# Optimization experiments

Hardware: AMD Instinct MI355X
Metric: run time of the kernel (lower is better)

The kernel has to match this reference:

```python
import jax, jax.numpy as jnp
import numpy as np

B, T, D, H = 256, 200, 128, 128


def setup_inputs() -> dict:
    key = jax.random.key(0)
    ks = jax.random.split(key, 6)
    return {
        "x": jax.random.normal(ks[0], (B, T, D), dtype=jnp.float32),
        "duration": jax.random.uniform(ks[1], (B, T), dtype=jnp.float32),
        "rep_indicies": jax.random.randint(ks[2], (B,), 0, T),
        "W_x": jax.random.normal(ks[3], (D, 7 * H), dtype=jnp.float32) / np.float32(np.sqrt(D)),
        "W_h": jax.random.normal(ks[4], (H, 7 * H), dtype=jnp.float32) / np.float32(np.sqrt(H)),
        "b": jnp.zeros((7 * H,), dtype=jnp.float32),
    }


def _ctlstm(x, duration, W_x, W_h, b):
    # Neural-Hawkes continuous-time LSTM scan. x:[B,T,D], duration:[B,T]
    xg = jnp.einsum("btd,dg->btg", x, W_x) + b  # [B,T,7H] precomputed input gates

    def step(carry, inputs):
        h, c_t, cbar = carry  # each [B,H]
        xg_t, dt = inputs     # [B,7H], [B]
        g = xg_t + h @ W_h
        i, f, z, o, ibar, fbar, d = jnp.split(g, 7, axis=-1)
        i, f, o = jax.nn.sigmoid(i), jax.nn.sigmoid(f), jax.nn.sigmoid(o)
        ibar, fbar = jax.nn.sigmoid(ibar), jax.nn.sigmoid(fbar)
        z = jnp.tanh(z)
        delta = jax.nn.softplus(d)
        c = f * c_t + i * z               # cell right after the event
        cbar_new = fbar * cbar + ibar * z  # target cell it decays toward
        c_new = cbar_new + (c - cbar_new) * jnp.exp(-delta * dt[:, None])
        h_new = o * jnp.tanh(c_new)
        return (h_new, c_new, cbar_new), (h_new, c_new)

    z0 = jnp.zeros((x.shape[0], W_h.shape[0]), dtype=x.dtype)
    _, (h_seq, c_seq) = jax.lax.scan(
        step, (z0, z0, z0), (jnp.swapaxes(xg, 0, 1), jnp.swapaxes(duration, 0, 1))
    )
    # h_seq/c_seq: [T,B,H] -> [B,T,H]
    return jnp.swapaxes(h_seq, 0, 1), jnp.swapaxes(c_seq, 0, 1)


def _gather_state(s, rep_indicies):
    # s:[B,T,H]; pick per-sample time index -> [1,B,H]
    idx = jnp.broadcast_to(rep_indicies[:, None, None], (s.shape[0], 1, s.shape[2]))
    return jnp.take_along_axis(s, idx, axis=1)[:, 0, :][None]


def reference(x, duration, rep_indicies, W_x, W_h, b):
    # Dropout is identity in eval mode.
    h_seq, c_seq = _ctlstm(x, duration, W_x, W_h, b)
    return (_gather_state(h_seq, rep_indicies), _gather_state(c_seq, rep_indicies))
```

## Files before the change

### kernel.cpp

```cpp
#include <hip/hip_runtime.h>

#define TT 200
#define BB 256
#define DD 128
#define HH 128
#define NG 896
#define NGP 1024
#define NGP2 1032
#define CH 16

typedef _Float16 half8 __attribute__((ext_vector_type(8)));
typedef _Float16 half4 __attribute__((ext_vector_type(4)));
typedef float float4v __attribute__((ext_vector_type(4)));
typedef int int4v __attribute__((ext_vector_type(4)));

__device__ __forceinline__ float rcpf_(float x) { return __builtin_amdgcn_rcpf(x); }
__device__ __forceinline__ float sigmoidf_(float x) { return rcpf_(1.f + __expf(-x)); }
__device__ __forceinline__ float tanhf_(float x) { return 1.f - 2.f * rcpf_(__expf(2.f * x) + 1.f); }
__device__ __forceinline__ float softplusf_(float x) {
  return fmaxf(x, 0.f) + 0.69314718056f * __log2f(1.f + __expf(-fabsf(x)));
}

__global__ __launch_bounds__(256) void prep_k(const float* __restrict__ Wx,
    const float* __restrict__ Wh, _Float16* __restrict__ WxTp,
    char* __restrict__ WhQ, float* __restrict__ wscale) {
  int bx = blockIdx.x, tid = threadIdx.x;
  if (bx < 28) {
    __shared__ _Float16 Tld[32][136];
    int j0 = bx * 32;
    int jo = tid & 31, kb = tid >> 5;
#pragma unroll
    for (int it = 0; it < 16; ++it) {
      int k = kb + it * 8;
      Tld[jo][k] = (_Float16)Wx[(size_t)k * NG + j0 + jo];
    }
    __syncthreads();
    int g = j0 >> 7, u0 = j0 & 127;
    int jw = tid >> 3, kq = (tid & 7) * 16;
    int pcol = (u0 + jw) * 8 + g;
    *(half8*)&WxTp[(size_t)pcol * DD + kq] = *(const half8*)&Tld[jw][kq];
    *(half8*)&WxTp[(size_t)pcol * DD + kq + 8] = *(const half8*)&Tld[jw][kq + 8];
    return;
  }
  __shared__ float redmax[4][64];
  int c = tid & 63, kq = tid >> 6;
  int col = (bx - 28) * 64 + c;
  float v[32];
  float m = 0.f;
#pragma unroll
  for (int i = 0; i < 32; ++i) {
    v[i] = Wh[(size_t)(kq * 32 + i) * NG + col];
    m = fmaxf(m, fabsf(v[i]));
  }
  redmax[kq][c] = m;
  __syncthreads();
  float mm = fmaxf(fmaxf(redmax[0][c], redmax[1][c]),
                   fmaxf(redmax[2][c], redmax[3][c]));
  mm = mm > 0.f ? mm : 1.f;
  float inv = 127.f * rcpf_(mm);
  char q[32];
#pragma unroll
  for (int i = 0; i < 32; ++i) q[i] = (char)__float2int_rn(v[i] * inv);
#pragma unroll
  for (int i = 0; i < 8; ++i)
    *(int*)&WhQ[(size_t)col * DD + kq * 32 + i * 4] = *(int*)&q[i * 4];
  if (kq == 0) wscale[col] = mm * (1.f / 127.f);
}

__global__ __launch_bounds__(512, 2) void rec_k(const float* __restrict__ x,
    const float* __restrict__ dur, const int* __restrict__ rep,
    const _Float16* __restrict__ WxTp, const char* __restrict__ WhQ,
    const float* __restrict__ wscale, const float* __restrict__ bias,
    float* __restrict__ out) {
  int b = blockIdx.x, j = threadIdx.x;
  int tend = rep[b];
  __shared__ __align__(16) _Float16 xgL[2][CH][NGP2];
  __shared__ __align__(16) _Float16 xld[CH][DD + 8];
  __shared__ __align__(16) char hq[2][HH];
  __shared__ float dlds[TT];
  int w = j >> 6, l = j & 63, lr = l & 15, lg = l >> 4;
  int u = w * 16 + lr;

  int4v wbq[7][2];
  half8 wbx[7][4];
  float sg[7], bias_r[7];
#pragma unroll
  for (int g = 0; g < 7; ++g) {
#pragma unroll
    for (int m = 0; m < 2; ++m)
      wbq[g][m] = *(const int4v*)(WhQ + (size_t)(g * HH + u) * DD + m * 64 + lg * 16);
#pragma unroll
    for (int kk = 0; kk < 4; ++kk)
      wbx[g][kk] = *(const half8*)(WxTp + ((size_t)u * 8 + g) * DD + kk * 32 + lg * 8);
    sg[g] = wscale[g * HH + u] * (1.f / 127.f);
    bias_r[g] = bias[g * HH + u];
  }
  for (int i = j; i < TT; i += 512) dlds[i] = dur[b * TT + i];
  if (lg == 0) { hq[0][u] = (char)0; hq[1][u] = (char)0; }
  float c_s = 0.f, cb_s = 0.f;

  int srow = j >> 5, skq = (j & 31) << 2;
  half8 af[4];
  half8 xo0 = {}, xo1 = {}, xo2 = {}, xo3 = {};
  float4v xraw = (float4v){0.f, 0.f, 0.f, 0.f};

#define PRODG(G)                                                                 \
  do {                                                                           \
    float bv = bias_r[(G)];                                                      \
    float4v pacc = (float4v){bv, bv, bv, bv};                                    \
    _Pragma("unroll") for (int kk = 0; kk < 4; ++kk)                             \
        pacc = __builtin_amdgcn_mfma_f32_16x16x32_f16(af[kk], wbx[(G)][kk],      \
                                                      pacc, 0, 0, 0);            \
    xo0[(G)] = (_Float16)pacc[0];                                                \
    xo1[(G)] = (_Float16)pacc[1];                                                \
    xo2[(G)] = (_Float16)pacc[2];                                                \
    xo3[(G)] = (_Float16)pacc[3];                                                \
  } while (0)

#define XO_WRITE(DST)                                                            \
  do {                                                                           \
    *(half8*)((DST) + (lg * 4 + 0) * NGP2 + u * 8) = xo0;                        \
    *(half8*)((DST) + (lg * 4 + 1) * NGP2 + u * 8) = xo1;                        \
    *(half8*)((DST) + (lg * 4 + 2) * NGP2 + u * 8) = xo2;                        \
    *(half8*)((DST) + (lg * 4 + 3) * NGP2 + u * 8) = xo3;                        \
  } while (0)

  {
    float4v xv = *(const float4v*)(x + ((size_t)b * TT + srow) * DD + skq);
    half4 h4 = {(_Float16)xv[0], (_Float16)xv[1], (_Float16)xv[2], (_Float16)xv[3]};
    *(half4*)&xld[srow][skq] = h4;
  }
  __syncthreads();
#pragma unroll
  for (int kk = 0; kk < 4; ++kk) af[kk] = *(const half8*)&xld[lr][kk * 32 + lg * 8];
  PRODG(0); PRODG(1); PRODG(2); PRODG(3); PRODG(4); PRODG(5); PRODG(6);
  XO_WRITE(&xgL[0][0][0]);
  __syncthreads();

#define PSLICE(S)                                                                \
  do {                                                                           \
    if ((S) == 0) {                                                              \
      int tr = min(base + CH + srow, TT - 1);                                    \
      xraw = *(const float4v*)(x + ((size_t)b * TT + tr) * DD + skq);            \
    } else if ((S) == 1) {                                                       \
      half4 h4 = {(_Float16)xraw[0], (_Float16)xraw[1],                          \
                  (_Float16)xraw[2], (_Float16)xraw[3]};                         \
      *(half4*)&xld[srow][skq] = h4;                                             \
    } else if ((S) == 2) {                                                       \
      _Pragma("unroll") for (int kk = 0; kk < 4; ++kk)                           \
          af[kk] = *(const half8*)&xld[lr][kk * 32 + lg * 8];                    \
    } else if ((S) >= 3 && (S) <= 9) {                                           \
      PRODG((S) - 3);                                                            \
    } else if ((S) == 10) {                                                      \
      XO_WRITE(nb_xg);                                                           \
    }                                                                            \
  } while (0)

#define FSTEP(S)                                                                 \
  if ((S) <= smax) {                                                             \
    if (hasNext) PSLICE(S);                                                      \
    int T = base + (S);                                                          \
    half8 xv = *(const half8*)(cb_xg + (S) * NGP2 + u * 8);                      \
    float dt = dlds[T];                                                          \
    const char* hin = hq[(S) & 1];                                               \
    char* hout = hq[((S) & 1) ^ 1];                                              \
    int4v aq0 = *(const int4v*)&hin[lg * 16];                                    \
    int4v aq1 = *(const int4v*)&hin[64 + lg * 16];                               \
    int4v acc[7];                                                                \
    _Pragma("unroll") for (int g = 0; g < 7; ++g) acc[g] = (int4v){0, 0, 0, 0};  \
    _Pragma("unroll") for (int g = 0; g < 7; ++g)                                \
        acc[g] = __builtin_amdgcn_mfma_i32_16x16x64_i8(aq0, wbq[g][0], acc[g], 0, 0, 0); \
    _Pragma("unroll") for (int g = 0; g < 7; ++g)                                \
        acc[g] = __builtin_amdgcn_mfma_i32_16x16x64_i8(aq1, wbq[g][1], acc[g], 0, 0, 0); \
    float gv[7];                                                                 \
    _Pragma("unroll") for (int g = 0; g < 7; ++g)                                \
        gv[g] = (float)acc[g][0] * sg[g] + (float)xv[g];                         \
    float iv = sigmoidf_(gv[0]), fv = sigmoidf_(gv[1]);                          \
    float zv = tanhf_(gv[2]), ov = sigmoidf_(gv[3]);                             \
    float ibv = sigmoidf_(gv[4]), fbv = sigmoidf_(gv[5]);                        \
    float dv = softplusf_(gv[6]);                                                \
    float cc = fv * c_s + iv * zv;                                               \
    cb_s = fbv * cb_s + ibv * zv;                                                \
    float cn = cb_s + (cc - cb_s) * __expf(-dv * dt);                            \
    float hn = ov * tanhf_(cn);                                                  \
    c_s = cn;                                                                    \
    char hb = (char)__float2int_rn(hn * 127.f);                                  \
    if (lg == 0) {                                                               \
      if (T == tend) {                                                           \
        out[b * HH + u] = hn;                                                    \
        out[BB * HH + b * HH + u] = cn;                                          \
      }                                                                          \
      hout[u] = hb;                                                              \
    }                                                                            \
    __syncthreads();                                                             \
  }

  for (int base = 0; base <= tend; base += CH) {
    int smax = min(CH - 1, tend - base);
    int hasNext = (base + CH) <= tend;
    const _Float16* cb_xg = &xgL[(base >> 4) & 1][0][0];
    _Float16* nb_xg = &xgL[((base >> 4) & 1) ^ 1][0][0];
    FSTEP(0)  FSTEP(1)  FSTEP(2)  FSTEP(3)
    FSTEP(4)  FSTEP(5)  FSTEP(6)  FSTEP(7)
    FSTEP(8)  FSTEP(9)  FSTEP(10) FSTEP(11)
    FSTEP(12) FSTEP(13) FSTEP(14) FSTEP(15)
  }
#undef FSTEP
#undef PSLICE
#undef XO_WRITE
#undef PRODG
}

extern "C" void kernel_launch(void* const* d_in, const int* in_sizes, int n_in,
                              void* d_out, int out_size, void* d_ws, size_t ws_size,
                              hipStream_t stream) {
  const float* x = (const float*)d_in[0];
  const float* dur = (const float*)d_in[1];
  const int* rep = (const int*)d_in[2];
  const float* Wx = (const float*)d_in[3];
  const float* Wh = (const float*)d_in[4];
  const float* bias = (const float*)d_in[5];
  float* out = (float*)d_out;
  char* ws = (char*)d_ws;

  size_t off = 0;
  _Float16* WxTp = (_Float16*)(ws + off); off += (size_t)NGP * DD * 2;
  char* WhQ = (char*)(ws + off); off += (size_t)NG * DD;
  off = (off + 255) & ~(size_t)255;
  float* wscale = (float*)(ws + off); off += (size_t)NG * 4;

  hipLaunchKernelGGL(prep_k, dim3(28 + NG / 64), dim3(256), 0, stream,
                     Wx, Wh, WxTp, WhQ, wscale);
  hipLaunchKernelGGL(rec_k, dim3(BB), dim3(512), 0, stream,
                     x, dur, rep, WxTp, WhQ, wscale, bias, out);
}
```

Before: 162.9 us.

## Stream W_x fragments from global per gate instead of holding them in registers

The 7x4 half8 W_x fragments are no longer kept resident in registers. Two double-buffered fragment sets are now reloaded from global memory (L2-cached) and prefetched one gate ahead inside the pipelined per-step slices. The recurrent int8 MFMA accumulators are also split into a 4-gate and a 3-gate group to shorten register live ranges. The aim is to cut VGPR pressure so the 512x2 launch bound holds without spilling, at the cost of extra global loads on each chunk.

Result: faster. 156.2 us (-4.2%).

```diff
diff --git a/kernel.cpp b/kernel.cpp
--- a/kernel.cpp
+++ b/kernel.cpp
@@ -82,16 +82,12 @@
   int u = w * 16 + lr;
 
   int4v wbq[7][2];
-  half8 wbx[7][4];
   float sg[7], bias_r[7];
 #pragma unroll
   for (int g = 0; g < 7; ++g) {
 #pragma unroll
     for (int m = 0; m < 2; ++m)
       wbq[g][m] = *(const int4v*)(WhQ + (size_t)(g * HH + u) * DD + m * 64 + lg * 16);
-#pragma unroll
-    for (int kk = 0; kk < 4; ++kk)
-      wbx[g][kk] = *(const half8*)(WxTp + ((size_t)u * 8 + g) * DD + kk * 32 + lg * 8);
     sg[g] = wscale[g * HH + u] * (1.f / 127.f);
     bias_r[g] = bias[g * HH + u];
   }
@@ -101,15 +97,23 @@
 
   int srow = j >> 5, skq = (j & 31) << 2;
   half8 af[4];
+  half8 bf0[4], bf1[4];
   half8 xo0 = {}, xo1 = {}, xo2 = {}, xo3 = {};
   float4v xraw = (float4v){0.f, 0.f, 0.f, 0.f};
 
-#define PRODG(G)                                                                 \
+#define WXLOAD(G, BUF)                                                           \
+  do {                                                                           \
+    _Pragma("unroll") for (int kk = 0; kk < 4; ++kk)                             \
+        BUF[kk] = *(const half8*)(WxTp + ((size_t)u * 8 + (G)) * DD +            \
+                                  kk * 32 + lg * 8);                             \
+  } while (0)
+
+#define PRODG(G, BUF)                                                            \
   do {                                                                           \
     float bv = bias_r[(G)];                                                      \
     float4v pacc = (float4v){bv, bv, bv, bv};                                    \
     _Pragma("unroll") for (int kk = 0; kk < 4; ++kk)                             \
-        pacc = __builtin_amdgcn_mfma_f32_16x16x32_f16(af[kk], wbx[(G)][kk],      \
+        pacc = __builtin_amdgcn_mfma_f32_16x16x32_f16(af[kk], BUF[kk],           \
                                                       pacc, 0, 0, 0);            \
     xo0[(G)] = (_Float16)pacc[0];                                                \
     xo1[(G)] = (_Float16)pacc[1];                                                \
@@ -133,7 +137,13 @@
   __syncthreads();
 #pragma unroll
   for (int kk = 0; kk < 4; ++kk) af[kk] = *(const half8*)&xld[lr][kk * 32 + lg * 8];
-  PRODG(0); PRODG(1); PRODG(2); PRODG(3); PRODG(4); PRODG(5); PRODG(6);
+  WXLOAD(0, bf0); PRODG(0, bf0);
+  WXLOAD(1, bf1); PRODG(1, bf1);
+  WXLOAD(2, bf0); PRODG(2, bf0);
+  WXLOAD(3, bf1); PRODG(3, bf1);
+  WXLOAD(4, bf0); PRODG(4, bf0);
+  WXLOAD(5, bf1); PRODG(5, bf1);
+  WXLOAD(6, bf0); PRODG(6, bf0);
   XO_WRITE(&xgL[0][0][0]);
   __syncthreads();
 
@@ -149,8 +159,15 @@
     } else if ((S) == 2) {                                                       \
       _Pragma("unroll") for (int kk = 0; kk < 4; ++kk)                           \
           af[kk] = *(const half8*)&xld[lr][kk * 32 + lg * 8];                    \
+      WXLOAD(0, bf1);                                                            \
     } else if ((S) >= 3 && (S) <= 9) {                                           \
-      PRODG((S) - 3);                                                            \
+      if (((S) & 1) == 1) {                                                      \
+        PRODG((S) - 3, bf1);                                                     \
+        if ((S) <= 8) WXLOAD((S) - 2, bf0);                                      \
+      } else {                                                                   \
+        PRODG((S) - 3, bf0);                                                     \
+        if ((S) <= 8) WXLOAD((S) - 2, bf1);                                      \
+      }                                                                          \
     } else if ((S) == 10) {                                                      \
       XO_WRITE(nb_xg);                                                           \
     }                                                                            \
@@ -166,15 +183,27 @@
     char* hout = hq[((S) & 1) ^ 1];                                              \
     int4v aq0 = *(const int4v*)&hin[lg * 16];                                    \
     int4v aq1 = *(const int4v*)&hin[64 + lg * 16];                               \
-    int4v acc[7];                                                                \
-    _Pragma("unroll") for (int g = 0; g < 7; ++g) acc[g] = (int4v){0, 0, 0, 0};  \
-    _Pragma("unroll") for (int g = 0; g < 7; ++g)                                \
+    float gv[7];                                                                 \
+    {                                                                            \
+      int4v acc[4];                                                              \
+      _Pragma("unroll") for (int g = 0; g < 4; ++g) {                            \
+        acc[g] = (int4v){0, 0, 0, 0};                                            \
         acc[g] = __builtin_amdgcn_mfma_i32_16x16x64_i8(aq0, wbq[g][0], acc[g], 0, 0, 0); \
-    _Pragma("unroll") for (int g = 0; g < 7; ++g)                                \
         acc[g] = __builtin_amdgcn_mfma_i32_16x16x64_i8(aq1, wbq[g][1], acc[g], 0, 0, 0); \
-    float gv[7];                                                                 \
-    _Pragma("unroll") for (int g = 0; g < 7; ++g)                                \
-        gv[g] = (float)acc[g][0] * sg[g] + (float)xv[g];                         \
+      }                                                                          \
+      _Pragma("unroll") for (int g = 0; g < 4; ++g)                              \
+          gv[g] = (float)acc[g][0] * sg[g] + (float)xv[g];                       \
+    }                                                                            \
+    {                                                                            \
+      int4v acc[3];                                                              \
+      _Pragma("unroll") for (int g = 0; g < 3; ++g) {                            \
+        acc[g] = (int4v){0, 0, 0, 0};                                            \
+        acc[g] = __builtin_amdgcn_mfma_i32_16x16x64_i8(aq0, wbq[g + 4][0], acc[g], 0, 0, 0); \
+        acc[g] = __builtin_amdgcn_mfma_i32_16x16x64_i8(aq1, wbq[g + 4][1], acc[g], 0, 0, 0); \
+      }                                                                          \
+      _Pragma("unroll") for (int g = 0; g < 3; ++g)                              \
+          gv[g + 4] = (float)acc[g][0] * sg[g + 4] + (float)xv[g + 4];           \
+    }                                                                            \
     float iv = sigmoidf_(gv[0]), fv = sigmoidf_(gv[1]);                          \
     float zv = tanhf_(gv[2]), ov = sigmoidf_(gv[3]);                             \
     float ibv = sigmoidf_(gv[4]), fbv = sigmoidf_(gv[5]);                        \
@@ -209,6 +238,7 @@
 #undef PSLICE
 #undef XO_WRITE
 #undef PRODG
+#undef WXLOAD
 }
 
 extern "C" void kernel_launch(void* const* d_in, const int* in_sizes, int n_in,
```
